# Kernel tuning notes

Hardware: AMD Instinct MI355X
Metric: run time of the kernel (lower is better)

Reference implementation:

```python
import jax, jax.numpy as jnp
import numpy as np


def setup_inputs() -> dict:
    key = jax.random.key(0)
    ks = jax.random.split(key, 4)
    B, H, W, C = 4, 64, 64, 256
    Ck = C // 8
    x = jax.random.normal(ks[0], (B, H, W, C), dtype=jnp.float32)
    Wf = jax.random.normal(ks[1], (C, Ck), dtype=jnp.float32) * (1.0 / np.sqrt(C))
    Wg = jax.random.normal(ks[2], (C, Ck), dtype=jnp.float32) * (1.0 / np.sqrt(C))
    Wh = jax.random.normal(ks[3], (C, C), dtype=jnp.float32) * (1.0 / np.sqrt(C))
    bf = jnp.zeros((Ck,), jnp.float32)
    bg = jnp.zeros((Ck,), jnp.float32)
    bh = jnp.zeros((C,), jnp.float32)
    gamma = jnp.ones((1,), jnp.float32)
    return {"x": x, "Wf": Wf, "bf": bf, "Wg": Wg, "bg": bg, "Wh": Wh, "bh": bh, "gamma": gamma}


def reference(x, Wf, bf, Wg, bg, Wh, bh, gamma):
    B, H, W, C = x.shape
    N = H * W
    xf = x.reshape(B, N, C)  # hw_flatten; 1x1 conv == per-pixel matmul
    f = xf @ Wf + bf          # [B, N, C//8] (keys)
    g = xf @ Wg + bg          # [B, N, C//8] (queries)
    h = xf @ Wh + bh          # [B, N, C]    (values)
    s = jnp.einsum('bnk,bmk->bnm', g, f)   # [B, N, N], no scaling (as in source)
    b = jax.nn.softmax(s, axis=-1)
    o = jnp.einsum('bnm,bmc->bnc', b, h)   # [B, N, C]
    y = gamma * o.reshape(B, H, W, C) + x
    return y
```

## Files before the change

kernel.cpp:

```cpp
#include <hip/hip_runtime.h>
#include <stdint.h>

typedef short short8 __attribute__((ext_vector_type(8)));
typedef short short4_t __attribute__((ext_vector_type(4)));
typedef float f32x4 __attribute__((ext_vector_type(4)));

__device__ __forceinline__ float bf2f(unsigned short u) {
    union { unsigned int i; float f; } v; v.i = ((unsigned int)u) << 16; return v.f;
}
__device__ __forceinline__ unsigned short f2bf(float f) {
    union { float f; unsigned int i; } v; v.f = f;
    return (unsigned short)((v.i + 0x8000u) >> 16);
}

__global__ __launch_bounds__(256) void k_prew(const float* __restrict__ Wf,
                                              const float* __restrict__ Wg,
                                              const float* __restrict__ Wh,
                                              unsigned short* __restrict__ wTh,
                                              unsigned short* __restrict__ wTl) {
    int col = blockIdx.x;
    int k = threadIdx.x;
    float v;
    if (col < 32) v = Wf[k * 32 + col];
    else if (col < 64) v = Wg[k * 32 + (col - 32)];
    else v = Wh[k * 256 + (col - 64)];
    unsigned short h = f2bf(v);
    wTh[col * 256 + k] = h;
    if (col < 64) wTl[col * 256 + k] = f2bf(v - bf2f(h));
}

__global__ __launch_bounds__(256) void k_proj(
    const float* __restrict__ x,
    const unsigned short* __restrict__ wTh,
    const unsigned short* __restrict__ wTl,
    const float* __restrict__ bfb,
    const float* __restrict__ bgb,
    const float* __restrict__ bhb,
    unsigned short* __restrict__ fKh,
    unsigned short* __restrict__ fKl,
    unsigned short* __restrict__ gQh,
    unsigned short* __restrict__ gQl,
    unsigned short* __restrict__ hT) {
    __shared__ short sm[4 * 64 * 72];
    int tid = threadIdx.x;
    int wave = tid >> 6, lane = tid & 63, lq = lane & 15, quad = lane >> 4;
    int rt = blockIdx.x;
    const float* xb = x + (size_t)rt * 64 * 256;
    f32x4 zero4 = {0.f, 0.f, 0.f, 0.f};

    if (blockIdx.y < 4) {
        const int XO = 0, WO = 64 * 136;
        int cb = blockIdx.y;
        const unsigned short* wbase = wTh + (size_t)(64 + cb * 64) * 256;
        f32x4 acc[4] = {zero4, zero4, zero4, zero4};

        for (int ph = 0; ph < 2; ++ph) {
            int k0 = ph * 128;
            __syncthreads();
#pragma unroll
            for (int u = 0; u < 4; ++u) {
                int q = u * 256 + tid;
                int row = q >> 4, kc = q & 15;
                const float* xs = &xb[row * 256 + k0 + kc * 8];
                f32x4 a0 = *(const f32x4*)xs;
                f32x4 a1 = *(const f32x4*)(xs + 4);
                short8 sh;
#pragma unroll
                for (int j = 0; j < 4; ++j) {
                    sh[j] = (short)f2bf(a0[j]);
                    sh[4 + j] = (short)f2bf(a1[j]);
                }
                *(short8*)&sm[XO + row * 136 + kc * 8] = sh;
                *(short8*)&sm[WO + row * 136 + kc * 8] =
                    *(const short8*)&wbase[row * 256 + k0 + kc * 8];
            }
            __syncthreads();
#pragma unroll
            for (int ks = 0; ks < 4; ++ks) {
                short8 a = *(const short8*)&sm[XO + (wave * 16 + lq) * 136 + ks * 32 + quad * 8];
#pragma unroll
                for (int ct = 0; ct < 4; ++ct) {
                    short8 bfr = *(const short8*)&sm[WO + (lq + 16 * ct) * 136 + ks * 32 + quad * 8];
                    acc[ct] = __builtin_amdgcn_mfma_f32_16x16x32_bf16(a, bfr, acc[ct], 0, 0, 0);
                }
            }
        }

        int rowl = wave * 16 + quad * 4;
        int grow0 = rt * 64;
        int bidx = grow0 >> 12, n0 = (grow0 & 4095) + rowl;
#pragma unroll
        for (int ct = 0; ct < 4; ++ct) {
            int c = cb * 64 + lq + 16 * ct;
            float bias = bhb[c];
            short4_t pk;
#pragma unroll
            for (int r = 0; r < 4; ++r) pk[r] = (short)f2bf(acc[ct][r] + bias);
            size_t a8 = (((size_t)(bidx * 16 + (c >> 4)) * 128 + (n0 >> 5)) * 64 +
                         ((n0 & 31) >> 3) * 16 + (c & 15)) * 8 + (n0 & 7);
            *(short4_t*)&hT[a8] = pk;
        }
    } else {
        const int XH = 0, XL = 64 * 72, WH = 2 * 64 * 72, WL = 3 * 64 * 72;
        f32x4 acc[4] = {zero4, zero4, zero4, zero4};

        for (int ph = 0; ph < 4; ++ph) {
            int k0 = ph * 64;
            __syncthreads();
#pragma unroll
            for (int u = 0; u < 2; ++u) {
                int q = u * 256 + tid;
                int row = q >> 3, kc = q & 7;
                const float* xs = &xb[row * 256 + k0 + kc * 8];
                f32x4 a0 = *(const f32x4*)xs;
                f32x4 a1 = *(const f32x4*)(xs + 4);
                short8 sh, sl;
#pragma unroll
                for (int j = 0; j < 4; ++j) {
                    unsigned short h0 = f2bf(a0[j]);
                    sh[j] = (short)h0; sl[j] = (short)f2bf(a0[j] - bf2f(h0));
                    unsigned short h1 = f2bf(a1[j]);
                    sh[4 + j] = (short)h1; sl[4 + j] = (short)f2bf(a1[j] - bf2f(h1));
                }
                *(short8*)&sm[XH + row * 72 + kc * 8] = sh;
                *(short8*)&sm[XL + row * 72 + kc * 8] = sl;
                *(short8*)&sm[WH + row * 72 + kc * 8] =
                    *(const short8*)&wTh[row * 256 + k0 + kc * 8];
                *(short8*)&sm[WL + row * 72 + kc * 8] =
                    *(const short8*)&wTl[row * 256 + k0 + kc * 8];
            }
            __syncthreads();
#pragma unroll
            for (int ks = 0; ks < 2; ++ks) {
                short8 ah = *(const short8*)&sm[XH + (wave * 16 + lq) * 72 + ks * 32 + quad * 8];
                short8 al = *(const short8*)&sm[XL + (wave * 16 + lq) * 72 + ks * 32 + quad * 8];
#pragma unroll
                for (int ct = 0; ct < 4; ++ct) {
                    short8 bh = *(const short8*)&sm[WH + (lq + 16 * ct) * 72 + ks * 32 + quad * 8];
                    short8 bl = *(const short8*)&sm[WL + (lq + 16 * ct) * 72 + ks * 32 + quad * 8];
                    acc[ct] = __builtin_amdgcn_mfma_f32_16x16x32_bf16(ah, bh, acc[ct], 0, 0, 0);
                    acc[ct] = __builtin_amdgcn_mfma_f32_16x16x32_bf16(al, bh, acc[ct], 0, 0, 0);
                    acc[ct] = __builtin_amdgcn_mfma_f32_16x16x32_bf16(ah, bl, acc[ct], 0, 0, 0);
                }
            }
        }

        int rowl = wave * 16 + quad * 4;
#pragma unroll
        for (int ct = 0; ct < 4; ++ct) {
            int coll = lq + 16 * ct;
#pragma unroll
            for (int r = 0; r < 4; ++r) {
                int grow = rt * 64 + rowl + r;
                int bidx = grow >> 12, n = grow & 4095;
                float v = acc[ct][r];
                size_t o = (size_t)(bidx * 256 + (n >> 4)) * 512 +
                           (((coll & 31) >> 3) * 16 + (n & 15)) * 8 + (coll & 7);
                if (coll < 32) {
                    v += bfb[coll];
                    unsigned short h = f2bf(v);
                    fKh[o] = h;
                    fKl[o] = f2bf(v - bf2f(h));
                } else {
                    int cg = coll - 32;
                    size_t og = (size_t)(bidx * 256 + (n >> 4)) * 512 +
                                ((cg >> 3) * 16 + (n & 15)) * 8 + (cg & 7);
                    v += bgb[cg];
                    unsigned short h = f2bf(v);
                    gQh[og] = h;
                    gQl[og] = f2bf(v - bf2f(h));
                }
            }
        }
    }
}

#define PSTR 72
__global__ __launch_bounds__(512, 4) void k_attn(
    const unsigned short* __restrict__ fKh,
    const unsigned short* __restrict__ fKl,
    const unsigned short* __restrict__ gQh,
    const unsigned short* __restrict__ gQl,
    const unsigned short* __restrict__ hT,
    float* __restrict__ pacc0,
    float* __restrict__ pacc1,
    float* __restrict__ pl) {
    __shared__ short Ps[2][64 * PSTR];
    __shared__ short Fb[2][2][2048];
    __shared__ float Lred[4][16][2];
    int tid = threadIdx.x;
    int wave = tid >> 6, lane = tid & 63, lq = lane & 15, quad = lane >> 4;
    int b = blockIdx.x & 3;
    int rest = blockIdx.x >> 2;
    int qt = rest & 63;
    int ks = rest >> 6;
    int rs = wave >> 1;
    int kh = wave & 1;
    int lchunk = quad * 16 + lq;

    const unsigned short* fhB = fKh + (size_t)b * 131072;
    const unsigned short* flB = fKl + (size_t)b * 131072;
    const unsigned short* hB  = hT + (size_t)b * 1048576;
    float* pacc = ks ? pacc1 : pacc0;
    float* plb  = pl + ks * 16384;

    f32x4 zero4 = {0.f, 0.f, 0.f, 0.f};
    f32x4 acc[8];
#pragma unroll
    for (int i = 0; i < 8; ++i) acc[i] = zero4;
    float l_part[4] = {0.f, 0.f, 0.f, 0.f};

    int gtile = b * 256 + qt * 4 + rs;
    short8 ghfrag = *(const short8*)&gQh[(size_t)gtile * 512 + lchunk * 8];
    short8 glfrag = *(const short8*)&gQl[(size_t)gtile * 512 + lchunk * 8];

    int sid = tid & 255;
    int hl = tid >> 8;
    const unsigned short* fB0 = hl ? flB : fhB;
    int ft0 = ks * 128;

    *(short8*)&Fb[0][hl][sid * 8] = *(const short8*)&fB0[(size_t)ft0 * 512 + sid * 8];
    __syncthreads();

    for (int kt = 0; kt < 32; ++kt) {
        int p = kt & 1;
        int nft = ft0 + (kt < 31 ? kt + 1 : kt) * 4;
        short8 fn = *(const short8*)&fB0[(size_t)nft * 512 + sid * 8];

        int k0 = ks * 64 + kt * 2;
        int ct0 = wave * 2;
        short8 hb00 = *(const short8*)&hB[(((size_t)(ct0 + 0) * 128 + k0 + 0) * 64 + lchunk) * 8];
        short8 hb01 = *(const short8*)&hB[(((size_t)(ct0 + 0) * 128 + k0 + 1) * 64 + lchunk) * 8];
        short8 hb10 = *(const short8*)&hB[(((size_t)(ct0 + 1) * 128 + k0 + 0) * 64 + lchunk) * 8];
        short8 hb11 = *(const short8*)&hB[(((size_t)(ct0 + 1) * 128 + k0 + 1) * 64 + lchunk) * 8];

        short8 fh0 = *(const short8*)&Fb[p][0][(kh * 2 + 0) * 512 + lchunk * 8];
        short8 fl0 = *(const short8*)&Fb[p][1][(kh * 2 + 0) * 512 + lchunk * 8];
        short8 fh1 = *(const short8*)&Fb[p][0][(kh * 2 + 1) * 512 + lchunk * 8];
        short8 fl1 = *(const short8*)&Fb[p][1][(kh * 2 + 1) * 512 + lchunk * 8];
        f32x4 S0 = __builtin_amdgcn_mfma_f32_16x16x32_bf16(ghfrag, fh0, zero4, 0, 0, 0);
        f32x4 S1 = __builtin_amdgcn_mfma_f32_16x16x32_bf16(ghfrag, fh1, zero4, 0, 0, 0);
        S0 = __builtin_amdgcn_mfma_f32_16x16x32_bf16(glfrag, fh0, S0, 0, 0, 0);
        S1 = __builtin_amdgcn_mfma_f32_16x16x32_bf16(glfrag, fh1, S1, 0, 0, 0);
        S0 = __builtin_amdgcn_mfma_f32_16x16x32_bf16(ghfrag, fl0, S0, 0, 0, 0);
        S1 = __builtin_amdgcn_mfma_f32_16x16x32_bf16(ghfrag, fl1, S1, 0, 0, 0);

#pragma unroll
        for (int r = 0; r < 4; ++r) {
            S0[r] = __expf(S0[r]);
            S1[r] = __expf(S1[r]);
            l_part[r] += S0[r] + S1[r];
        }
#pragma unroll
        for (int r = 0; r < 4; ++r) {
            int row = rs * 16 + quad * 4 + r;
            Ps[p][row * PSTR + (kh * 2 + 0) * 16 + lq] = (short)f2bf(S0[r]);
            Ps[p][row * PSTR + (kh * 2 + 1) * 16 + lq] = (short)f2bf(S1[r]);
        }

        *(short8*)&Fb[1 - p][hl][sid * 8] = fn;

        __syncthreads();

#pragma unroll
        for (int rb = 0; rb < 4; ++rb) {
            short8 pa0 = *(const short8*)&Ps[p][(rb * 16 + lq) * PSTR + quad * 8];
            short8 pa1 = *(const short8*)&Ps[p][(rb * 16 + lq) * PSTR + 32 + quad * 8];
            acc[rb * 2 + 0] = __builtin_amdgcn_mfma_f32_16x16x32_bf16(pa0, hb00, acc[rb * 2 + 0], 0, 0, 0);
            acc[rb * 2 + 0] = __builtin_amdgcn_mfma_f32_16x16x32_bf16(pa1, hb01, acc[rb * 2 + 0], 0, 0, 0);
            acc[rb * 2 + 1] = __builtin_amdgcn_mfma_f32_16x16x32_bf16(pa0, hb10, acc[rb * 2 + 1], 0, 0, 0);
            acc[rb * 2 + 1] = __builtin_amdgcn_mfma_f32_16x16x32_bf16(pa1, hb11, acc[rb * 2 + 1], 0, 0, 0);
        }
    }

#pragma unroll
    for (int r = 0; r < 4; ++r) {
        float s = l_part[r];
        s += __shfl_xor(s, 1);
        s += __shfl_xor(s, 2);
        s += __shfl_xor(s, 4);
        s += __shfl_xor(s, 8);
        if (lq == 0) Lred[rs][quad * 4 + r][kh] = s;
    }
    __syncthreads();
    if (kh == 0 && lq == 0) {
#pragma unroll
        for (int r = 0; r < 4; ++r) {
            int rl = quad * 4 + r;
            plb[b * 4096 + qt * 64 + rs * 16 + rl] = Lred[rs][rl][0] + Lred[rs][rl][1];
        }
    }

#pragma unroll
    for (int rb = 0; rb < 4; ++rb)
#pragma unroll
        for (int ct = 0; ct < 2; ++ct) {
            int c = wave * 32 + ct * 16 + lq;
#pragma unroll
            for (int r = 0; r < 4; ++r) {
                int n = qt * 64 + rb * 16 + quad * 4 + r;
                pacc[((size_t)(b * 4096 + n)) * 256 + c] = acc[rb * 2 + ct][r];
            }
        }
}

__global__ __launch_bounds__(256) void k_combine(
    const float* __restrict__ x,
    const float* __restrict__ gam_p,
    const float* __restrict__ pacc1,
    const float* __restrict__ pl,
    float* __restrict__ out) {
    int gid = blockIdx.x * 256 + threadIdx.x;
    int row = gid >> 6;
    f32x4 a0 = *(const f32x4*)&out[(size_t)gid * 4];
    f32x4 a1 = *(const f32x4*)&pacc1[(size_t)gid * 4];
    f32x4 xv = *(const f32x4*)&x[(size_t)gid * 4];
    float linv = 1.0f / (pl[row] + pl[16384 + row]);
    float gam = gam_p[0];
    f32x4 o;
#pragma unroll
    for (int j = 0; j < 4; ++j) o[j] = gam * ((a0[j] + a1[j]) * linv) + xv[j];
    *(f32x4*)&out[(size_t)gid * 4] = o;
}

extern "C" void kernel_launch(void* const* d_in, const int* in_sizes, int n_in,
                              void* d_out, int out_size, void* d_ws, size_t ws_size,
                              hipStream_t stream) {
    const float* x   = (const float*)d_in[0];
    const float* Wf  = (const float*)d_in[1];
    const float* bfb = (const float*)d_in[2];
    const float* Wg  = (const float*)d_in[3];
    const float* bgb = (const float*)d_in[4];
    const float* Wh  = (const float*)d_in[5];
    const float* bhb = (const float*)d_in[6];
    const float* gam = (const float*)d_in[7];
    float* out = (float*)d_out;

    char* ws = (char*)d_ws;
    const size_t MI = 1u << 20;
    unsigned short* fKh = (unsigned short*)(ws);
    unsigned short* fKl = (unsigned short*)(ws + 1 * MI);
    unsigned short* gQh = (unsigned short*)(ws + 2 * MI);
    unsigned short* gQl = (unsigned short*)(ws + 3 * MI);
    unsigned short* hT  = (unsigned short*)(ws + 4 * MI);
    unsigned short* wTh = (unsigned short*)(ws + 12 * MI);
    unsigned short* wTl = (unsigned short*)(ws + 12 * MI + 160 * 1024);
    float* pacc1 = (float*)(ws + 13 * MI);
    float* pl    = (float*)(ws + 29 * MI);

    k_prew<<<dim3(320), dim3(256), 0, stream>>>(Wf, Wg, Wh, wTh, wTl);
    k_proj<<<dim3(256, 5), dim3(256), 0, stream>>>(x, wTh, wTl, bfb, bgb, bhb,
                                                   fKh, fKl, gQh, gQl, hT);
    k_attn<<<dim3(512), dim3(512), 0, stream>>>(fKh, fKl, gQh, gQl, hT,
                                                out, pacc1, pl);
    k_combine<<<dim3(4096), dim3(256), 0, stream>>>(x, gam, pacc1, pl, out);
}
```

Measured before the change: 154.1 us.

## Fuse weight prep into projection and combine into attention via atomic ticket

Removes the separate weight-transpose kernel: the projection kernel now reads fp32 weights directly and converts/transposes them into shared memory. The value projection covers 128 columns per block, so there are 3 y-blocks instead of 5. The combine kernel is also removed: each attention block takes an atomic ticket, and the second of each split-K pair reads its partner's partial sums and normaliser and writes the final output. This saves two launches and an extra pass over the partial buffers, at the cost of redundant weight conversion in every block, an added memset, and reliance on threadfence/atomic ordering.

```diff
diff --git a/kernel.cpp b/kernel.cpp
--- a/kernel.cpp
+++ b/kernel.cpp
@@ -13,26 +13,11 @@
     return (unsigned short)((v.i + 0x8000u) >> 16);
 }
 
-__global__ __launch_bounds__(256) void k_prew(const float* __restrict__ Wf,
-                                              const float* __restrict__ Wg,
-                                              const float* __restrict__ Wh,
-                                              unsigned short* __restrict__ wTh,
-                                              unsigned short* __restrict__ wTl) {
-    int col = blockIdx.x;
-    int k = threadIdx.x;
-    float v;
-    if (col < 32) v = Wf[k * 32 + col];
-    else if (col < 64) v = Wg[k * 32 + (col - 32)];
-    else v = Wh[k * 256 + (col - 64)];
-    unsigned short h = f2bf(v);
-    wTh[col * 256 + k] = h;
-    if (col < 64) wTl[col * 256 + k] = f2bf(v - bf2f(h));
-}
-
 __global__ __launch_bounds__(256) void k_proj(
     const float* __restrict__ x,
-    const unsigned short* __restrict__ wTh,
-    const unsigned short* __restrict__ wTl,
+    const float* __restrict__ Wf,
+    const float* __restrict__ Wg,
+    const float* __restrict__ Wh,
     const float* __restrict__ bfb,
     const float* __restrict__ bgb,
     const float* __restrict__ bhb,
@@ -41,18 +26,19 @@
     unsigned short* __restrict__ gQh,
     unsigned short* __restrict__ gQl,
     unsigned short* __restrict__ hT) {
-    __shared__ short sm[4 * 64 * 72];
+    __shared__ short sm[26496];
     int tid = threadIdx.x;
     int wave = tid >> 6, lane = tid & 63, lq = lane & 15, quad = lane >> 4;
     int rt = blockIdx.x;
     const float* xb = x + (size_t)rt * 64 * 256;
     f32x4 zero4 = {0.f, 0.f, 0.f, 0.f};
 
-    if (blockIdx.y < 4) {
-        const int XO = 0, WO = 64 * 136;
+    if (blockIdx.y < 2) {
+        const int XO = 0, WO = 64 * 138;
         int cb = blockIdx.y;
-        const unsigned short* wbase = wTh + (size_t)(64 + cb * 64) * 256;
-        f32x4 acc[4] = {zero4, zero4, zero4, zero4};
+        f32x4 acc[8];
+#pragma unroll
+        for (int i = 0; i < 8; ++i) acc[i] = zero4;
 
         for (int ph = 0; ph < 2; ++ph) {
             int k0 = ph * 128;
@@ -70,17 +56,33 @@
                     sh[j] = (short)f2bf(a0[j]);
                     sh[4 + j] = (short)f2bf(a1[j]);
                 }
-                *(short8*)&sm[XO + row * 136 + kc * 8] = sh;
-                *(short8*)&sm[WO + row * 136 + kc * 8] =
-                    *(const short8*)&wbase[row * 256 + k0 + kc * 8];
+                *(short8*)&sm[XO + row * 138 + kc * 8] = sh;
+            }
+            {
+                int c4 = (tid & 31) * 4;
+                int seg = tid >> 5;
+#pragma unroll
+                for (int jj = 0; jj < 2; ++jj) {
+                    f32x4 v[8];
+#pragma unroll
+                    for (int j = 0; j < 8; ++j)
+                        v[j] = *(const f32x4*)&Wh[(size_t)(k0 + seg * 16 + jj * 8 + j) * 256 + cb * 128 + c4];
+#pragma unroll
+                    for (int i = 0; i < 4; ++i) {
+                        short8 w;
+#pragma unroll
+                        for (int j = 0; j < 8; ++j) w[j] = (short)f2bf(v[j][i]);
+                        *(short8*)&sm[WO + (c4 + i) * 138 + seg * 16 + jj * 8] = w;
+                    }
+                }
             }
             __syncthreads();
 #pragma unroll
             for (int ks = 0; ks < 4; ++ks) {
-                short8 a = *(const short8*)&sm[XO + (wave * 16 + lq) * 136 + ks * 32 + quad * 8];
-#pragma unroll
-                for (int ct = 0; ct < 4; ++ct) {
-                    short8 bfr = *(const short8*)&sm[WO + (lq + 16 * ct) * 136 + ks * 32 + quad * 8];
+                short8 a = *(const short8*)&sm[XO + (wave * 16 + lq) * 138 + ks * 32 + quad * 8];
+#pragma unroll
+                for (int ct = 0; ct < 8; ++ct) {
+                    short8 bfr = *(const short8*)&sm[WO + (lq + 16 * ct) * 138 + ks * 32 + quad * 8];
                     acc[ct] = __builtin_amdgcn_mfma_f32_16x16x32_bf16(a, bfr, acc[ct], 0, 0, 0);
                 }
             }
@@ -90,8 +92,8 @@
         int grow0 = rt * 64;
         int bidx = grow0 >> 12, n0 = (grow0 & 4095) + rowl;
 #pragma unroll
-        for (int ct = 0; ct < 4; ++ct) {
-            int c = cb * 64 + lq + 16 * ct;
+        for (int ct = 0; ct < 8; ++ct) {
+            int c = cb * 128 + lq + 16 * ct;
             float bias = bhb[c];
             short4_t pk;
 #pragma unroll
@@ -101,7 +103,7 @@
             *(short4_t*)&hT[a8] = pk;
         }
     } else {
-        const int XH = 0, XL = 64 * 72, WH = 2 * 64 * 72, WL = 3 * 64 * 72;
+        const int XH = 0, XL = 4608, WH = 9216, WL = 13824;
         f32x4 acc[4] = {zero4, zero4, zero4, zero4};
 
         for (int ph = 0; ph < 4; ++ph) {
@@ -124,10 +126,27 @@
                 }
                 *(short8*)&sm[XH + row * 72 + kc * 8] = sh;
                 *(short8*)&sm[XL + row * 72 + kc * 8] = sl;
-                *(short8*)&sm[WH + row * 72 + kc * 8] =
-                    *(const short8*)&wTh[row * 256 + k0 + kc * 8];
-                *(short8*)&sm[WL + row * 72 + kc * 8] =
-                    *(const short8*)&wTl[row * 256 + k0 + kc * 8];
+            }
+            {
+                int c_loc = tid & 63;
+                int seg = tid >> 6;
+                const float* wsrc = (c_loc < 32) ? &Wf[c_loc] : &Wg[c_loc - 32];
+#pragma unroll
+                for (int jj = 0; jj < 2; ++jj) {
+                    float v[8];
+#pragma unroll
+                    for (int j = 0; j < 8; ++j)
+                        v[j] = wsrc[(size_t)(k0 + seg * 16 + jj * 8 + j) * 32];
+                    short8 shh, sll;
+#pragma unroll
+                    for (int j = 0; j < 8; ++j) {
+                        unsigned short h = f2bf(v[j]);
+                        shh[j] = (short)h;
+                        sll[j] = (short)f2bf(v[j] - bf2f(h));
+                    }
+                    *(short8*)&sm[WH + c_loc * 72 + seg * 16 + jj * 8] = shh;
+                    *(short8*)&sm[WL + c_loc * 72 + seg * 16 + jj * 8] = sll;
+                }
             }
             __syncthreads();
 #pragma unroll
@@ -182,12 +201,16 @@
     const unsigned short* __restrict__ gQh,
     const unsigned short* __restrict__ gQl,
     const unsigned short* __restrict__ hT,
-    float* __restrict__ pacc0,
+    const float* __restrict__ x,
+    const float* __restrict__ gam_p,
+    float* __restrict__ out,
     float* __restrict__ pacc1,
-    float* __restrict__ pl) {
+    float* __restrict__ pl,
+    int* __restrict__ flags) {
     __shared__ short Ps[2][64 * PSTR];
     __shared__ short Fb[2][2][2048];
     __shared__ float Lred[4][16][2];
+    __shared__ int tick_s;
     int tid = threadIdx.x;
     int wave = tid >> 6, lane = tid & 63, lq = lane & 15, quad = lane >> 4;
     int b = blockIdx.x & 3;
@@ -201,8 +224,6 @@
     const unsigned short* fhB = fKh + (size_t)b * 131072;
     const unsigned short* flB = fKl + (size_t)b * 131072;
     const unsigned short* hB  = hT + (size_t)b * 1048576;
-    float* pacc = ks ? pacc1 : pacc0;
-    float* plb  = pl + ks * 16384;
 
     f32x4 zero4 = {0.f, 0.f, 0.f, 0.f};
     f32x4 acc[8];
@@ -287,10 +308,12 @@
 #pragma unroll
         for (int r = 0; r < 4; ++r) {
             int rl = quad * 4 + r;
-            plb[b * 4096 + qt * 64 + rs * 16 + rl] = Lred[rs][rl][0] + Lred[rs][rl][1];
+            pl[ks * 16384 + b * 4096 + qt * 64 + rs * 16 + rl] =
+                Lred[rs][rl][0] + Lred[rs][rl][1];
         }
     }
 
+    float* mypart = ks ? pacc1 : out;
 #pragma unroll
     for (int rb = 0; rb < 4; ++rb)
 #pragma unroll
@@ -299,28 +322,35 @@
 #pragma unroll
             for (int r = 0; r < 4; ++r) {
                 int n = qt * 64 + rb * 16 + quad * 4 + r;
-                pacc[((size_t)(b * 4096 + n)) * 256 + c] = acc[rb * 2 + ct][r];
-            }
-        }
-}
-
-__global__ __launch_bounds__(256) void k_combine(
-    const float* __restrict__ x,
-    const float* __restrict__ gam_p,
-    const float* __restrict__ pacc1,
-    const float* __restrict__ pl,
-    float* __restrict__ out) {
-    int gid = blockIdx.x * 256 + threadIdx.x;
-    int row = gid >> 6;
-    f32x4 a0 = *(const f32x4*)&out[(size_t)gid * 4];
-    f32x4 a1 = *(const f32x4*)&pacc1[(size_t)gid * 4];
-    f32x4 xv = *(const f32x4*)&x[(size_t)gid * 4];
-    float linv = 1.0f / (pl[row] + pl[16384 + row]);
+                mypart[((size_t)(b * 4096 + n)) * 256 + c] = acc[rb * 2 + ct][r];
+            }
+        }
+
+    __threadfence();
+    __syncthreads();
+    if (tid == 0) tick_s = atomicAdd(&flags[blockIdx.x & 255], 1);
+    __syncthreads();
+    if (tick_s == 0) return;
+    __threadfence();
+
+    const float* opart = ks ? out : pacc1;
+    const float* plp = &pl[(size_t)(1 - ks) * 16384 + b * 4096 + qt * 64];
     float gam = gam_p[0];
-    f32x4 o;
-#pragma unroll
-    for (int j = 0; j < 4; ++j) o[j] = gam * ((a0[j] + a1[j]) * linv) + xv[j];
-    *(f32x4*)&out[(size_t)gid * 4] = o;
+#pragma unroll
+    for (int rb = 0; rb < 4; ++rb)
+#pragma unroll
+        for (int r = 0; r < 4; ++r) {
+            int row_loc = rb * 16 + quad * 4 + r;
+            float l = (Lred[rb][quad * 4 + r][0] + Lred[rb][quad * 4 + r][1]) + plp[row_loc];
+            float linv = 1.0f / l;
+            size_t rowo = ((size_t)(b * 4096 + qt * 64 + row_loc)) * 256;
+#pragma unroll
+            for (int ct = 0; ct < 2; ++ct) {
+                int c = wave * 32 + ct * 16 + lq;
+                float o = acc[rb * 2 + ct][r] + opart[rowo + c];
+                out[rowo + c] = gam * o * linv + x[rowo + c];
+            }
+        }
 }
 
 extern "C" void kernel_launch(void* const* d_in, const int* in_sizes, int n_in,
@@ -343,15 +373,13 @@
     unsigned short* gQh = (unsigned short*)(ws + 2 * MI);
     unsigned short* gQl = (unsigned short*)(ws + 3 * MI);
     unsigned short* hT  = (unsigned short*)(ws + 4 * MI);
-    unsigned short* wTh = (unsigned short*)(ws + 12 * MI);
-    unsigned short* wTl = (unsigned short*)(ws + 12 * MI + 160 * 1024);
-    float* pacc1 = (float*)(ws + 13 * MI);
-    float* pl    = (float*)(ws + 29 * MI);
-
-    k_prew<<<dim3(320), dim3(256), 0, stream>>>(Wf, Wg, Wh, wTh, wTl);
-    k_proj<<<dim3(256, 5), dim3(256), 0, stream>>>(x, wTh, wTl, bfb, bgb, bhb,
+    float* pacc1 = (float*)(ws + 12 * MI);
+    float* pl    = (float*)(ws + 28 * MI);
+    int*   flags = (int*)(ws + 28 * MI + 128 * 1024);
+
+    hipMemsetAsync(flags, 0, 256 * sizeof(int), stream);
+    k_proj<<<dim3(256, 3), dim3(256), 0, stream>>>(x, Wf, Wg, Wh, bfb, bgb, bhb,
                                                    fKh, fKl, gQh, gQl, hT);
     k_attn<<<dim3(512), dim3(512), 0, stream>>>(fKh, fKl, gQh, gQl, hT,
-                                                out, pacc1, pl);
-    k_combine<<<dim3(4096), dim3(256), 0, stream>>>(x, gam, pacc1, pl, out);
-}
+                                                x, gam, out, pacc1, pl, flags);
+}
```

After: 323.1 us. 2.1x slower.
